# Kernel tuning notes

Measured on AMD Instinct MI355X. Metric: run time of the kernel, lower is better.

The kernel has to match this reference:

```python
import jax, jax.numpy as jnp
import numpy as np

N_NODES = 100000
N_EDGES = 3200000
IN_C = 256
OUT_C = 64
NEG_SLOPE = 0.2  # leaky_relu alpha


def setup_inputs() -> dict:
    key = jax.random.key(0)
    k1, k2, k3, k4 = jax.random.split(key, 4)
    x = jax.random.normal(k1, (N_NODES, IN_C), dtype=jnp.float32)
    edge_index = jax.random.randint(k2, (2, N_EDGES), 0, N_NODES, dtype=jnp.int32)
    # xavier-ish scales
    W = jax.random.normal(k3, (OUT_C, IN_C), dtype=jnp.float32) * (1.0 / np.sqrt(IN_C))
    a = jax.random.normal(k4, (2 * OUT_C, 1), dtype=jnp.float32) * 0.1
    return {"x": x, "edge_index": edge_index, "W": W, "a": a, "num_nodes": N_NODES}


def reference(x, edge_index, W, a, num_nodes):
    # eval mode: dropout is identity
    # add self loops
    loop = jnp.arange(num_nodes, dtype=edge_index.dtype)
    row = jnp.concatenate([edge_index[0], loop])  # source nodes (x_j)
    col = jnp.concatenate([edge_index[1], loop])  # destination nodes (x_i)

    h = x @ W.T  # [N, out_c]

    # e = cat([x_i, x_j], 1) @ a  ==  (h @ a_i)[col] + (h @ a_j)[row]
    a_i = a[:OUT_C, 0]
    a_j = a[OUT_C:, 0]
    s_i = h @ a_i  # [N]
    s_j = h @ a_j  # [N]
    e = jax.nn.leaky_relu(s_i[col] + s_j[row], negative_slope=NEG_SLOPE)  # [E+N]

    # segment softmax over destination node (col)
    m = jax.ops.segment_max(e, col, num_segments=num_nodes)  # [N]
    ex = jnp.exp(e - m[col])
    denom = jax.ops.segment_sum(ex, col, num_segments=num_nodes)  # [N]
    alpha = ex / denom[col]  # [E+N]

    # scatter-add aggregation: out[col] += alpha * h[row]
    out = jax.ops.segment_sum(alpha[:, None] * h[row], col, num_segments=num_nodes)
    return out
```

## Files before the change

kernel.cpp:

```cpp
#include <hip/hip_runtime.h>
#include <hip/hip_bf16.h>
#include <cstddef>
#include <cstdint>

#define IN_C 256
#define OUT_C 64
#define NEG_SLOPE 0.2f
#define BKT2 512
#define PCHUNK 4096
#define MAXB 256
#define CAP 18432

typedef __attribute__((ext_vector_type(4))) float f32x4;
typedef __attribute__((ext_vector_type(8))) short s16x8;

__device__ __forceinline__ float lrelu_exp(float t)
{
    t = (t >= 0.f) ? t : NEG_SLOPE * t;
    return __expf(t);
}

__device__ __forceinline__ float bf2f(ushort u)
{
    return __uint_as_float(((uint32_t)u) << 16);
}

__device__ __forceinline__ ushort f2bf(float f)
{
    uint32_t u = __float_as_uint(f);
    u += 0x7fffu + ((u >> 16) & 1u);
    return (ushort)(u >> 16);
}

__device__ __forceinline__ uint32_t pack_bf2(float f0, float f1)
{
    const uint32_t u0 = __float_as_uint(f0) + 0x8000u;
    const uint32_t u1 = __float_as_uint(f1) + 0x8000u;
    return (u1 & 0xffff0000u) | (u0 >> 16);
}

__global__ __launch_bounds__(256) void wconv_kernel(
    const float* __restrict__ W, ushort* __restrict__ wfrag,
    int* __restrict__ cursor, int nb)
{
    if (blockIdx.x == 64) {
        const int i = threadIdx.x;
        if (i < nb) cursor[i] = i * CAP;
        return;
    }
    const int idx = blockIdx.x * 256 + threadIdx.x;
    const int j = idx & 7;
    const int l = (idx >> 3) & 63;
    const int n = (idx >> 9) & 3;
    const int t = idx >> 11;
    const int k   = t * 32 + ((l >> 4) << 3) + j;
    const int col = n * 16 + (l & 15);
    wfrag[idx] = f2bf(W[col * IN_C + k]);
}

__global__ __launch_bounds__(256) void fused_h_mfma(
    const float* __restrict__ x, const ushort* __restrict__ wfrag,
    const float* __restrict__ a, ushort* __restrict__ hb,
    float* __restrict__ s_i, float* __restrict__ s_j, int n_nodes)
{
    __shared__ ushort Bs[32 * 64 * 8];

    const int tid = threadIdx.x;
    for (int i = tid; i < 2048; i += 256)
        ((float4*)Bs)[i] = ((const float4*)wfrag)[i];
    __syncthreads();

    const int lane = tid & 63;
    const int wv   = tid >> 6;
    const int m    = lane & 15;
    const int quad = lane >> 4;

    const int base = blockIdx.x * 64 + wv * 16;
    int row = base + m;
    if (row >= n_nodes) row = n_nodes - 1;

    f32x4 acc0 = {0.f, 0.f, 0.f, 0.f};
    f32x4 acc1 = {0.f, 0.f, 0.f, 0.f};
    f32x4 acc2 = {0.f, 0.f, 0.f, 0.f};
    f32x4 acc3 = {0.f, 0.f, 0.f, 0.f};

    const float* xrow = x + (size_t)row * IN_C + quad * 8;

    #pragma unroll
    for (int t = 0; t < 8; ++t) {
        const float4 xa = *(const float4*)(xrow + t * 32);
        const float4 xb = *(const float4*)(xrow + t * 32 + 4);
        union { s16x8 v; uint32_t u[4]; } af;
        af.u[0] = pack_bf2(xa.x, xa.y);
        af.u[1] = pack_bf2(xa.z, xa.w);
        af.u[2] = pack_bf2(xb.x, xb.y);
        af.u[3] = pack_bf2(xb.z, xb.w);

        const s16x8 b0 = *(const s16x8*)(Bs + ((t * 4 + 0) * 64 + lane) * 8);
        const s16x8 b1 = *(const s16x8*)(Bs + ((t * 4 + 1) * 64 + lane) * 8);
        const s16x8 b2 = *(const s16x8*)(Bs + ((t * 4 + 2) * 64 + lane) * 8);
        const s16x8 b3 = *(const s16x8*)(Bs + ((t * 4 + 3) * 64 + lane) * 8);

        acc0 = __builtin_amdgcn_mfma_f32_16x16x32_bf16(af.v, b0, acc0, 0, 0, 0);
        acc1 = __builtin_amdgcn_mfma_f32_16x16x32_bf16(af.v, b1, acc1, 0, 0, 0);
        acc2 = __builtin_amdgcn_mfma_f32_16x16x32_bf16(af.v, b2, acc2, 0, 0, 0);
        acc3 = __builtin_amdgcn_mfma_f32_16x16x32_bf16(af.v, b3, acc3, 0, 0, 0);
    }

    const int c0 = lane & 15;
    const float ai0 = a[c0],      ai1 = a[c0 + 16], ai2 = a[c0 + 32], ai3 = a[c0 + 48];
    const float aj0 = a[64 + c0], aj1 = a[80 + c0], aj2 = a[96 + c0], aj3 = a[112 + c0];

    #pragma unroll
    for (int r = 0; r < 4; ++r) {
        const int rowr = base + quad * 4 + r;
        float pi = acc0[r] * ai0 + acc1[r] * ai1 + acc2[r] * ai2 + acc3[r] * ai3;
        float pj = acc0[r] * aj0 + acc1[r] * aj1 + acc2[r] * aj2 + acc3[r] * aj3;
        pi += __shfl_xor(pi, 1, 64);  pj += __shfl_xor(pj, 1, 64);
        pi += __shfl_xor(pi, 2, 64);  pj += __shfl_xor(pj, 2, 64);
        pi += __shfl_xor(pi, 4, 64);  pj += __shfl_xor(pj, 4, 64);
        pi += __shfl_xor(pi, 8, 64);  pj += __shfl_xor(pj, 8, 64);
        if (rowr < n_nodes) {
            ushort* hr = hb + (size_t)rowr * OUT_C + c0;
            hr[0]  = f2bf(acc0[r]);
            hr[16] = f2bf(acc1[r]);
            hr[32] = f2bf(acc2[r]);
            hr[48] = f2bf(acc3[r]);
            if (c0 == 0) { s_i[rowr] = pi; s_j[rowr] = pj; }
        }
    }
}

__global__ __launch_bounds__(256) void partition_kernel(
    const int* __restrict__ ei, int* __restrict__ cursor,
    uint32_t* __restrict__ rec, int n_edges, int nb)
{
    __shared__ int      hist[MAXB];
    __shared__ int      lbase[MAXB];
    __shared__ int      gbase[MAXB];
    __shared__ int      lcur[MAXB];
    __shared__ uint32_t srt[PCHUNK];
    __shared__ uint8_t  bmap[PCHUNK];

    const int tid  = threadIdx.x;
    const int base = blockIdx.x * PCHUNK;
    const int lim  = min(PCHUNK, n_edges - base);

    hist[tid] = 0;
    __syncthreads();

    int rA[PCHUNK / 256], cA[PCHUNK / 256];
    #pragma unroll
    for (int k = 0; k < PCHUNK / 256; ++k) {
        const int i = tid + (k << 8);
        if (i < lim) {
            rA[k] = ei[base + i];
            cA[k] = ei[n_edges + base + i];
            atomicAdd(&hist[(uint32_t)cA[k] >> 9], 1);
        }
    }
    __syncthreads();

    const int v = hist[tid];
    lbase[tid] = v;
    __syncthreads();
    for (int off = 1; off < 256; off <<= 1) {
        const int mine  = lbase[tid];
        const int other = (tid >= off) ? lbase[tid - off] : 0;
        __syncthreads();
        lbase[tid] = mine + other;
        __syncthreads();
    }
    const int excl = lbase[tid] - v;
    __syncthreads();
    lbase[tid] = excl;
    lcur[tid]  = excl;
    gbase[tid] = (tid < nb && v > 0) ? atomicAdd(&cursor[tid], v) : 0;
    __syncthreads();

    #pragma unroll
    for (int k = 0; k < PCHUNK / 256; ++k) {
        const int i = tid + (k << 8);
        if (i < lim) {
            const int r = rA[k];
            const int c = cA[k];
            const int b = (uint32_t)c >> 9;
            const int pos = atomicAdd(&lcur[b], 1);
            srt[pos]  = ((uint32_t)r << 9) | (uint32_t)(c & (BKT2 - 1));
            bmap[pos] = (uint8_t)b;
        }
    }
    __syncthreads();

    for (int i = tid; i < lim; i += 256) {
        const int b = bmap[i];
        rec[gbase[b] + (i - lbase[b])] = srt[i];
    }
}

__global__ __launch_bounds__(512) void refine_kernel(
    uint32_t* __restrict__ rec, const int* __restrict__ cursor,
    int* __restrict__ nodeoff, int n_nodes, int nb)
{
    __shared__ uint32_t recs[CAP];
    __shared__ uint32_t dst[CAP];
    __shared__ int hcnt[BKT2];
    __shared__ int lcur[BKT2];
    __shared__ int sscan[BKT2];

    const int b     = blockIdx.x;
    const int tid   = threadIdx.x;
    const int start = b * CAP;
    const int cnt   = min(cursor[b] - start, CAP);

    hcnt[tid] = 0;
    __syncthreads();

    for (int i = tid; i < cnt; i += 512) {
        const uint32_t rv = rec[start + i];
        recs[i] = rv;
        atomicAdd(&hcnt[rv & (BKT2 - 1)], 1);
    }
    __syncthreads();

    const int myc = hcnt[tid];
    sscan[tid] = myc;
    __syncthreads();
    for (int off = 1; off < 512; off <<= 1) {
        const int mine  = sscan[tid];
        const int other = (tid >= off) ? sscan[tid - off] : 0;
        __syncthreads();
        sscan[tid] = mine + other;
        __syncthreads();
    }
    const int excl = sscan[tid] - myc;
    lcur[tid] = excl;
    const int g = b * BKT2 + tid;
    if (g < n_nodes) nodeoff[g] = start + excl;
    if (b == nb - 1 && tid == 0) nodeoff[n_nodes] = start + cnt;
    __syncthreads();

    for (int i = tid; i < cnt; i += 512) {
        const uint32_t rv = recs[i];
        const int pos = atomicAdd(&lcur[rv & (BKT2 - 1)], 1);
        dst[pos] = rv;
    }
    __syncthreads();

    for (int i = tid; i < cnt; i += 512)
        rec[start + i] = dst[i];
}

__global__ __launch_bounds__(256) void gather_kernel(
    const uint32_t* __restrict__ rec, const ushort* __restrict__ hb,
    const float* __restrict__ s_i, const float* __restrict__ s_j,
    const int* __restrict__ nodeoff, const int* __restrict__ cursor,
    float* __restrict__ out, int n_nodes)
{
    int wid = (int)((blockIdx.x * 256u + threadIdx.x) >> 6);
    wid = __builtin_amdgcn_readfirstlane(wid);
    if (wid >= n_nodes) return;
    const int lane = threadIdx.x & 63;

    const int o = nodeoff[wid];
    int oe;
    if ((wid & (BKT2 - 1)) == BKT2 - 1) {
        const int b = wid >> 9;
        oe = min(cursor[b], b * CAP + CAP);
    } else {
        oe = nodeoff[wid + 1];
    }

    const float si = s_i[wid];

    const float ex0 = lrelu_exp(si + s_j[wid]);
    float acc  = ex0 * bf2f(hb[(size_t)wid * OUT_C + lane]);
    float dsum = ex0;

    int e = o;
    for (; e + 16 <= oe; e += 16) {
        uint32_t rv[16];
        #pragma unroll
        for (int q = 0; q < 16; ++q) rv[q] = rec[e + q];
        float hv[16], sj[16];
        #pragma unroll
        for (int q = 0; q < 16; ++q) {
            const int r = (int)(rv[q] >> 9);
            hv[q] = bf2f(hb[(size_t)r * OUT_C + lane]);
            sj[q] = s_j[r];
        }
        #pragma unroll
        for (int q = 0; q < 16; ++q) {
            const float ex = lrelu_exp(si + sj[q]);
            acc  += ex * hv[q];
            dsum += ex;
        }
    }
    for (; e + 4 <= oe; e += 4) {
        uint32_t rv[4];
        #pragma unroll
        for (int q = 0; q < 4; ++q) rv[q] = rec[e + q];
        float hv[4], sj[4];
        #pragma unroll
        for (int q = 0; q < 4; ++q) {
            const int r = (int)(rv[q] >> 9);
            hv[q] = bf2f(hb[(size_t)r * OUT_C + lane]);
            sj[q] = s_j[r];
        }
        #pragma unroll
        for (int q = 0; q < 4; ++q) {
            const float ex = lrelu_exp(si + sj[q]);
            acc  += ex * hv[q];
            dsum += ex;
        }
    }
    for (; e < oe; ++e) {
        const uint32_t rv = rec[e];
        const int r = (int)(rv >> 9);
        const float ex = lrelu_exp(si + s_j[r]);
        acc  += ex * bf2f(hb[(size_t)r * OUT_C + lane]);
        dsum += ex;
    }

    out[(size_t)wid * OUT_C + lane] = acc / dsum;
}

extern "C" void kernel_launch(void* const* d_in, const int* in_sizes, int n_in,
                              void* d_out, int out_size, void* d_ws, size_t ws_size,
                              hipStream_t stream)
{
    const float* x  = (const float*)d_in[0];
    const int*   ei = (const int*)d_in[1];
    const float* W  = (const float*)d_in[2];
    const float* a  = (const float*)d_in[3];

    const int N  = in_sizes[0] / IN_C;
    const int E  = in_sizes[1] / 2;
    const int NB = (N + BKT2 - 1) / BKT2;

    float* out = (float*)d_out;

    char* ws = (char*)d_ws;
    ushort* hb      = (ushort*)ws;                ws += (size_t)N * OUT_C * 2;
    float*  s_i     = (float*)ws;                 ws += (size_t)N * 4;
    float*  s_j     = (float*)ws;                 ws += (size_t)N * 4;
    int*    cursor  = (int*)ws;                   ws += (size_t)MAXB * 4;
    int*    nodeoff = (int*)ws;                   ws += (size_t)(N + 1) * 4;
    ws = (char*)(((uintptr_t)ws + 15) & ~(uintptr_t)15);
    ushort* wfrag   = (ushort*)ws;                ws += 32 * 64 * 8 * 2;
    ws = (char*)(((uintptr_t)ws + 15) & ~(uintptr_t)15);
    uint32_t* rec   = (uint32_t*)ws;

    hipLaunchKernelGGL(wconv_kernel, dim3(65), dim3(256), 0, stream,
                       W, wfrag, cursor, NB);
    hipLaunchKernelGGL(fused_h_mfma, dim3((N + 63) / 64), dim3(256), 0, stream,
                       x, wfrag, a, hb, s_i, s_j, N);

    const int pblocks = (E + PCHUNK - 1) / PCHUNK;
    hipLaunchKernelGGL(partition_kernel, dim3(pblocks), dim3(256), 0, stream,
                       ei, cursor, rec, E, NB);

    hipLaunchKernelGGL(refine_kernel, dim3(NB), dim3(512), 0, stream,
                       rec, cursor, nodeoff, N, NB);

    hipLaunchKernelGGL(gather_kernel, dim3((N + 3) / 4), dim3(256), 0, stream,
                       rec, hb, s_i, s_j, nodeoff, cursor, out, N);
}
```

Measured before the change: 311.8 us.

## Vectorize gather with 4 edges per wave and simplify refine scatter

```diff
diff --git a/kernel.cpp b/kernel.cpp
--- a/kernel.cpp
+++ b/kernel.cpp
@@ -198,12 +198,11 @@
     }
 }
 
-__global__ __launch_bounds__(512) void refine_kernel(
+__global__ __launch_bounds__(1024) void refine_kernel(
     uint32_t* __restrict__ rec, const int* __restrict__ cursor,
     int* __restrict__ nodeoff, int n_nodes, int nb)
 {
     __shared__ uint32_t recs[CAP];
-    __shared__ uint32_t dst[CAP];
     __shared__ int hcnt[BKT2];
     __shared__ int lcur[BKT2];
     __shared__ int sscan[BKT2];
@@ -213,42 +212,52 @@
     const int start = b * CAP;
     const int cnt   = min(cursor[b] - start, CAP);
 
-    hcnt[tid] = 0;
-    __syncthreads();
-
-    for (int i = tid; i < cnt; i += 512) {
+    if (tid < BKT2) hcnt[tid] = 0;
+    __syncthreads();
+
+    const int cnt4 = cnt >> 2;
+    for (int i = tid; i < cnt4; i += 1024) {
+        const uint4 rv4 = ((const uint4*)(rec + start))[i];
+        ((uint4*)recs)[i] = rv4;
+        atomicAdd(&hcnt[rv4.x & (BKT2 - 1)], 1);
+        atomicAdd(&hcnt[rv4.y & (BKT2 - 1)], 1);
+        atomicAdd(&hcnt[rv4.z & (BKT2 - 1)], 1);
+        atomicAdd(&hcnt[rv4.w & (BKT2 - 1)], 1);
+    }
+    for (int i = (cnt & ~3) + tid; i < cnt; i += 1024) {
         const uint32_t rv = rec[start + i];
         recs[i] = rv;
         atomicAdd(&hcnt[rv & (BKT2 - 1)], 1);
     }
     __syncthreads();
 
-    const int myc = hcnt[tid];
-    sscan[tid] = myc;
-    __syncthreads();
-    for (int off = 1; off < 512; off <<= 1) {
-        const int mine  = sscan[tid];
-        const int other = (tid >= off) ? sscan[tid - off] : 0;
+    if (tid < BKT2) sscan[tid] = hcnt[tid];
+    __syncthreads();
+    for (int off = 1; off < BKT2; off <<= 1) {
+        int mine = 0, other = 0;
+        if (tid < BKT2) {
+            mine  = sscan[tid];
+            other = (tid >= off) ? sscan[tid - off] : 0;
+        }
         __syncthreads();
-        sscan[tid] = mine + other;
+        if (tid < BKT2) sscan[tid] = mine + other;
         __syncthreads();
     }
-    const int excl = sscan[tid] - myc;
-    lcur[tid] = excl;
-    const int g = b * BKT2 + tid;
-    if (g < n_nodes) nodeoff[g] = start + excl;
+    if (tid < BKT2) {
+        const int myc  = hcnt[tid];
+        const int excl = sscan[tid] - myc;
+        lcur[tid] = excl;
+        const int g = b * BKT2 + tid;
+        if (g < n_nodes) nodeoff[g] = start + excl;
+    }
     if (b == nb - 1 && tid == 0) nodeoff[n_nodes] = start + cnt;
     __syncthreads();
 
-    for (int i = tid; i < cnt; i += 512) {
+    for (int i = tid; i < cnt; i += 1024) {
         const uint32_t rv = recs[i];
         const int pos = atomicAdd(&lcur[rv & (BKT2 - 1)], 1);
-        dst[pos] = rv;
-    }
-    __syncthreads();
-
-    for (int i = tid; i < cnt; i += 512)
-        rec[start + i] = dst[i];
+        rec[start + pos] = rv;
+    }
 }
 
 __global__ __launch_bounds__(256) void gather_kernel(
@@ -261,6 +270,9 @@
     wid = __builtin_amdgcn_readfirstlane(wid);
     if (wid >= n_nodes) return;
     const int lane = threadIdx.x & 63;
+    const int g    = lane >> 4;
+    const int l4   = lane & 15;
+    const uint32_t loff = (uint32_t)(l4 << 3);
 
     const int o = nodeoff[wid];
     int oe;
@@ -272,57 +284,85 @@
     }
 
     const float si = s_i[wid];
-
-    const float ex0 = lrelu_exp(si + s_j[wid]);
-    float acc  = ex0 * bf2f(hb[(size_t)wid * OUT_C + lane]);
-    float dsum = ex0;
+    const char* hbB = (const char*)hb;
+
+    f32x4 acc = {0.f, 0.f, 0.f, 0.f};
+    float dsum = 0.f;
 
     int e = o;
     for (; e + 16 <= oe; e += 16) {
-        uint32_t rv[16];
-        #pragma unroll
-        for (int q = 0; q < 16; ++q) rv[q] = rec[e + q];
-        float hv[16], sj[16];
-        #pragma unroll
-        for (int q = 0; q < 16; ++q) {
-            const int r = (int)(rv[q] >> 9);
-            hv[q] = bf2f(hb[(size_t)r * OUT_C + lane]);
-            sj[q] = s_j[r];
-        }
-        #pragma unroll
-        for (int q = 0; q < 16; ++q) {
-            const float ex = lrelu_exp(si + sj[q]);
-            acc  += ex * hv[q];
-            dsum += ex;
-        }
-    }
-    for (; e + 4 <= oe; e += 4) {
         uint32_t rv[4];
         #pragma unroll
-        for (int q = 0; q < 4; ++q) rv[q] = rec[e + q];
-        float hv[4], sj[4];
+        for (int q = 0; q < 4; ++q) rv[q] = rec[e + q * 4 + g];
+        float sj[4]; uint32_t off[4];
         #pragma unroll
         for (int q = 0; q < 4; ++q) {
-            const int r = (int)(rv[q] >> 9);
-            hv[q] = bf2f(hb[(size_t)r * OUT_C + lane]);
-            sj[q] = s_j[r];
-        }
+            sj[q]  = s_j[rv[q] >> 9];
+            off[q] = ((rv[q] & 0xFFFFFE00u) >> 2) + loff;
+        }
+        uint2 hv[4];
+        #pragma unroll
+        for (int q = 0; q < 4; ++q) hv[q] = *(const uint2*)(hbB + off[q]);
         #pragma unroll
         for (int q = 0; q < 4; ++q) {
             const float ex = lrelu_exp(si + sj[q]);
-            acc  += ex * hv[q];
+            acc[0] += ex * __uint_as_float(hv[q].x << 16);
+            acc[1] += ex * __uint_as_float(hv[q].x & 0xffff0000u);
+            acc[2] += ex * __uint_as_float(hv[q].y << 16);
+            acc[3] += ex * __uint_as_float(hv[q].y & 0xffff0000u);
             dsum += ex;
         }
     }
-    for (; e < oe; ++e) {
-        const uint32_t rv = rec[e];
-        const int r = (int)(rv >> 9);
-        const float ex = lrelu_exp(si + s_j[r]);
-        acc  += ex * bf2f(hb[(size_t)r * OUT_C + lane]);
+    for (; e + 4 <= oe; e += 4) {
+        const uint32_t rv = rec[e + g];
+        const float sj = s_j[rv >> 9];
+        const uint32_t off = ((rv & 0xFFFFFE00u) >> 2) + loff;
+        const uint2 hv = *(const uint2*)(hbB + off);
+        const float ex = lrelu_exp(si + sj);
+        acc[0] += ex * __uint_as_float(hv.x << 16);
+        acc[1] += ex * __uint_as_float(hv.x & 0xffff0000u);
+        acc[2] += ex * __uint_as_float(hv.y << 16);
+        acc[3] += ex * __uint_as_float(hv.y & 0xffff0000u);
         dsum += ex;
     }
-
-    out[(size_t)wid * OUT_C + lane] = acc / dsum;
+    if (e < oe) {
+        const int m = oe - e;
+        const uint32_t rv = rec[e + (g < m ? g : m - 1)];
+        const float sj = s_j[rv >> 9];
+        const uint32_t off = ((rv & 0xFFFFFE00u) >> 2) + loff;
+        const uint2 hv = *(const uint2*)(hbB + off);
+        const float ex = (g < m) ? lrelu_exp(si + sj) : 0.f;
+        acc[0] += ex * __uint_as_float(hv.x << 16);
+        acc[1] += ex * __uint_as_float(hv.x & 0xffff0000u);
+        acc[2] += ex * __uint_as_float(hv.y << 16);
+        acc[3] += ex * __uint_as_float(hv.y & 0xffff0000u);
+        dsum += ex;
+    }
+
+    #pragma unroll
+    for (int k = 0; k < 4; ++k) {
+        acc[k] += __shfl_xor(acc[k], 16, 64);
+        acc[k] += __shfl_xor(acc[k], 32, 64);
+    }
+    dsum += __shfl_xor(dsum, 16, 64);
+    dsum += __shfl_xor(dsum, 32, 64);
+
+    const float ex0 = lrelu_exp(si + s_j[wid]);
+    const uint2 hs = *(const uint2*)(hbB + (size_t)wid * 128 + loff);
+    acc[0] += ex0 * __uint_as_float(hs.x << 16);
+    acc[1] += ex0 * __uint_as_float(hs.x & 0xffff0000u);
+    acc[2] += ex0 * __uint_as_float(hs.y << 16);
+    acc[3] += ex0 * __uint_as_float(hs.y & 0xffff0000u);
+    dsum += ex0;
+
+    if (g == 0) {
+        float4 o4;
+        o4.x = acc[0] / dsum;
+        o4.y = acc[1] / dsum;
+        o4.z = acc[2] / dsum;
+        o4.w = acc[3] / dsum;
+        *(float4*)(out + (size_t)wid * OUT_C + (l4 << 2)) = o4;
+    }
 }
 
 extern "C" void kernel_launch(void* const* d_in, const int* in_sizes, int n_in,
@@ -360,7 +400,7 @@
     hipLaunchKernelGGL(partition_kernel, dim3(pblocks), dim3(256), 0, stream,
                        ei, cursor, rec, E, NB);
 
-    hipLaunchKernelGGL(refine_kernel, dim3(NB), dim3(512), 0, stream,
+    hipLaunchKernelGGL(refine_kernel, dim3(NB), dim3(1024), 0, stream,
                        rec, cursor, nodeoff, N, NB);
 
     hipLaunchKernelGGL(gather_kernel, dim3((N + 3) / 4), dim3(256), 0, stream,
```

Measured after the change: 299.3 us. 1.04x faster.
